# Kernel optimization log

Measured on AMD Instinct MI355X. Metric: run time of the kernel, lower is better.

Reference implementation:

```python
import jax, jax.numpy as jnp
import numpy as np

B, N, D = 16, 4096, 768   # bags, instances per bag, feature dim
H, L, K = 12, 2, 16       # heads, MHA layers, topk
DH = D // H               # head dim (also gate hidden dim)


def _ln(x, g, b, eps=1e-5):
    m = x.mean(-1, keepdims=True)
    v = x.var(-1, keepdims=True)
    return (x - m) / jnp.sqrt(v + eps) * g + b


def setup_inputs() -> dict:
    key = jax.random.key(0)
    ks = jax.random.split(key, 8)
    s = 0.02
    return {
        "x": jax.random.normal(ks[0], (B, N, D), jnp.float32),
        "cls_token": jax.random.normal(ks[1], (1, 1, D), jnp.float32),
        "ln_g": jnp.ones((D,), jnp.float32),
        "ln_b": jnp.zeros((D,), jnp.float32),
        "gln_g": jnp.ones((D,), jnp.float32),
        "gln_b": jnp.zeros((D,), jnp.float32),
        "gW1": jax.random.normal(ks[2], (DH, D), jnp.float32) * s,
        "gb1": jnp.zeros((DH,), jnp.float32),
        "gW2": jax.random.normal(ks[3], (1, DH), jnp.float32) * s,
        "gb2": jnp.zeros((1,), jnp.float32),
        "Wqkv": jax.random.normal(ks[4], (L, 3 * D, D), jnp.float32) * s,
        "bqkv": jnp.zeros((L, 3 * D), jnp.float32),
        "Wo": jax.random.normal(ks[5], (L, D, D), jnp.float32) * s,
        "bo": jnp.zeros((L, D), jnp.float32),
    }


def reference(x, cls_token, ln_g, ln_b, gln_g, gln_b, gW1, gb1, gW2, gb2, Wqkv, bqkv, Wo, bo):
    # --- per-bag attention gate: LN -> Linear(D,DH) -> GELU -> Linear(DH,1) -> sigmoid ---
    z = _ln(x, gln_g, gln_b)                                      # [B,N,D]
    h = jax.nn.gelu(jnp.einsum('bnd,ed->bne', z, gW1) + gb1, approximate=False)
    w = jax.nn.sigmoid((jnp.einsum('bne,oe->bno', h, gW2) + gb2)[..., 0])  # [B,N]
    # --- top-k selection (argsort descending, take first K) + gather + weight ---
    topv, topi = jax.lax.top_k(w, K)                              # [B,K]
    sel = jnp.take_along_axis(x, topi[..., None], axis=1) * topv[..., None]  # [B,K,D]
    # --- prepend cls token, shared LayerNorm ---
    cls = jnp.broadcast_to(cls_token, (B, 1, D))
    seq = jnp.concatenate([cls, sel], axis=1)                     # [B,K+1,D]
    z0 = _ln(seq, ln_g, ln_b)
    a = z0
    S = K + 1
    scale = 1.0 / jnp.sqrt(jnp.asarray(DH, jnp.float32))
    # --- stacked MHA; residual always from z0, shared ln (matches source) ---
    for l in range(L):
        qkv = jnp.einsum('bsd,ed->bse', a, Wqkv[l]) + bqkv[l]     # [B,S,3D]
        q, k, v = jnp.split(qkv, 3, axis=-1)
        q = q.reshape(B, S, H, DH)
        k = k.reshape(B, S, H, DH)
        v = v.reshape(B, S, H, DH)
        att = jax.nn.softmax(jnp.einsum('bqhd,bkhd->bhqk', q, k) * scale, axis=-1)
        o = jnp.einsum('bhqk,bkhd->bqhd', att, v).reshape(B, S, D)
        o = jnp.einsum('bsd,ed->bse', o, Wo[l]) + bo[l]
        a = _ln(z0 + o, ln_g, ln_b)
    # dropout is identity in eval mode
    return a[:, 0, :]                                             # [B,D]
```

## Files before the change

### kernel.cpp

```cpp
#include <hip/hip_runtime.h>
#include <hip/hip_bf16.h>
#include <math.h>

#define B_   16
#define N_   4096
#define D_   768
#define H_   12
#define L_   2
#define K_   16
#define S_   17
#define M_   272
#define BN_  65536

typedef __bf16 bf16x8 __attribute__((ext_vector_type(8)));
typedef float  f32x4  __attribute__((ext_vector_type(4)));

static __device__ __forceinline__ unsigned short f2bf(float f) {
    __bf16 h = (__bf16)f;
    return __builtin_bit_cast(unsigned short, h);
}
static __device__ __forceinline__ float bf2f(unsigned short u) {
    __bf16 h = __builtin_bit_cast(__bf16, u);
    return (float)h;
}
static __device__ __forceinline__ unsigned long long umax64(unsigned long long a, unsigned long long b) {
    return a > b ? a : b;
}

__global__ __launch_bounds__(256)
void gate_kernel(const float* __restrict__ x,
                 const float* __restrict__ gln_g,
                 const float* __restrict__ gln_b,
                 const float* __restrict__ gW1,
                 const float* __restrict__ gb1,
                 const float* __restrict__ gW2,
                 const float* __restrict__ gb2,
                 float* __restrict__ wbuf)
{
    __shared__ unsigned short smem[24576];
    unsigned short* Xh = smem;
    unsigned short* Xl = smem + 8192;
    unsigned short* Wh = smem + 16384;
    unsigned short* Wl = smem + 20480;
    char* XhB = (char*)Xh; char* XlB = (char*)Xl;
    char* WhB = (char*)Wh; char* WlB = (char*)Wl;

    const int t   = threadIdx.x;
    const int bn0 = blockIdx.x * 128;

    const int trow  = t >> 1;
    const int thalf = (t & 1) * 32;
    const int te    = t >> 2;
    const int tq    = (t & 3) * 16;

    const float* xrow = x + (size_t)(bn0 + trow) * D_ + thalf;
    const float* wrow = gW1 + (size_t)te * D_ + tq;

    const int wv = t >> 6;
    const int l  = t & 63;
    const int fr = l & 15;
    const int fq = l >> 4;

    f32x4 acc[2][4];
    #pragma unroll
    for (int mi = 0; mi < 2; ++mi)
        #pragma unroll
        for (int ni = 0; ni < 4; ++ni) {
            f32x4 z = {0.f, 0.f, 0.f, 0.f};
            acc[mi][ni] = z;
        }

    float sxp = 0.f, sxxp = 0.f;
    float a1p = 0.f, a2p = 0.f;

    for (int kt = 0; kt < 12; ++kt) {
        __syncthreads();
        const float* src = xrow + kt * 64;
        #pragma unroll
        for (int j = 0; j < 8; ++j) {
            float4 v = *(const float4*)(src + j * 4);
            sxp  += v.x + v.y + v.z + v.w;
            sxxp += v.x * v.x + v.y * v.y + v.z * v.z + v.w * v.w;
            ushort4 hh, ll;
            hh.x = f2bf(v.x); ll.x = f2bf(v.x - bf2f(hh.x));
            hh.y = f2bf(v.y); ll.y = f2bf(v.y - bf2f(hh.y));
            hh.z = f2bf(v.z); ll.z = f2bf(v.z - bf2f(hh.z));
            hh.w = f2bf(v.w); ll.w = f2bf(v.w - bf2f(hh.w));
            int byte = trow * 128 + (thalf + j * 4) * 2;
            int sw   = byte ^ ((trow & 7) << 4);
            *(ushort4*)(XhB + sw) = hh;
            *(ushort4*)(XlB + sw) = ll;
        }
        const float* wsrc = wrow + kt * 64;
        const float* gsrc = gln_g + kt * 64 + tq;
        const float* bsrc = gln_b + kt * 64 + tq;
        #pragma unroll
        for (int j = 0; j < 4; ++j) {
            float4 w4 = *(const float4*)(wsrc + j * 4);
            float4 g4 = *(const float4*)(gsrc + j * 4);
            float4 b4 = *(const float4*)(bsrc + j * 4);
            float4 wt;
            wt.x = w4.x * g4.x; wt.y = w4.y * g4.y;
            wt.z = w4.z * g4.z; wt.w = w4.w * g4.w;
            a1p += wt.x + wt.y + wt.z + wt.w;
            a2p += b4.x * w4.x + b4.y * w4.y + b4.z * w4.z + b4.w * w4.w;
            ushort4 hh, ll;
            hh.x = f2bf(wt.x); ll.x = f2bf(wt.x - bf2f(hh.x));
            hh.y = f2bf(wt.y); ll.y = f2bf(wt.y - bf2f(hh.y));
            hh.z = f2bf(wt.z); ll.z = f2bf(wt.z - bf2f(hh.z));
            hh.w = f2bf(wt.w); ll.w = f2bf(wt.w - bf2f(hh.w));
            int byte = te * 128 + (tq + j * 4) * 2;
            int sw   = byte ^ ((te & 7) << 4);
            *(ushort4*)(WhB + sw) = hh;
            *(ushort4*)(WlB + sw) = ll;
        }
        __syncthreads();
        #pragma unroll
        for (int ks = 0; ks < 2; ++ks) {
            int k0 = ks * 32 + fq * 8;
            bf16x8 ah[2], al[2], bh[4], bl[4];
            #pragma unroll
            for (int mi = 0; mi < 2; ++mi) {
                int r    = wv * 32 + mi * 16 + fr;
                int byte = (r * 128 + k0 * 2) ^ ((r & 7) << 4);
                ah[mi] = *(const bf16x8*)(XhB + byte);
                al[mi] = *(const bf16x8*)(XlB + byte);
            }
            #pragma unroll
            for (int ni = 0; ni < 4; ++ni) {
                int e    = ni * 16 + fr;
                int byte = (e * 128 + k0 * 2) ^ ((e & 7) << 4);
                bh[ni] = *(const bf16x8*)(WhB + byte);
                bl[ni] = *(const bf16x8*)(WlB + byte);
            }
            #pragma unroll
            for (int mi = 0; mi < 2; ++mi)
                #pragma unroll
                for (int ni = 0; ni < 4; ++ni) {
                    acc[mi][ni] = __builtin_amdgcn_mfma_f32_16x16x32_bf16(ah[mi], bh[ni], acc[mi][ni], 0, 0, 0);
                    acc[mi][ni] = __builtin_amdgcn_mfma_f32_16x16x32_bf16(ah[mi], bl[ni], acc[mi][ni], 0, 0, 0);
                    acc[mi][ni] = __builtin_amdgcn_mfma_f32_16x16x32_bf16(al[mi], bh[ni], acc[mi][ni], 0, 0, 0);
                }
        }
    }
    __syncthreads();

    float* F    = (float*)smem;
    float* mS   = F;
    float* rS   = F + 128;
    float* A1s  = F + 256;
    float* A2s  = F + 320;
    float* redS = F + 384;
    float* redQ = F + 640;
    float* rA1  = F + 896;
    float* rA2  = F + 1152;

    redS[trow * 2 + (t & 1)] = sxp;
    redQ[trow * 2 + (t & 1)] = sxxp;
    rA1[te * 4 + (t & 3)] = a1p;
    rA2[te * 4 + (t & 3)] = a2p;
    __syncthreads();
    if (t < 128) {
        float s = redS[t * 2] + redS[t * 2 + 1];
        float q = redQ[t * 2] + redQ[t * 2 + 1];
        float m = s * (1.0f / D_);
        mS[t] = m;
        rS[t] = rsqrtf(q * (1.0f / D_) - m * m + 1e-5f);
    }
    if (t < 64) {
        A1s[t] = rA1[t * 4] + rA1[t * 4 + 1] + rA1[t * 4 + 2] + rA1[t * 4 + 3];
        A2s[t] = rA2[t * 4] + rA2[t * 4 + 1] + rA2[t * 4 + 2] + rA2[t * 4 + 3];
    }
    __syncthreads();

    float w2v[4], a1v[4], a2b[4];
    #pragma unroll
    for (int ni = 0; ni < 4; ++ni) {
        int e = ni * 16 + fr;
        w2v[ni] = gW2[e];
        a1v[ni] = A1s[e];
        a2b[ni] = A2s[e] + gb1[e];
    }
    float gb2v = gb2[0];

    #pragma unroll
    for (int mi = 0; mi < 2; ++mi) {
        #pragma unroll
        for (int j = 0; j < 4; ++j) {
            int inst = wv * 32 + mi * 16 + fq * 4 + j;
            float m = mS[inst], rs = rS[inst];
            float tp = 0.f;
            #pragma unroll
            for (int ni = 0; ni < 4; ++ni) {
                float h  = rs * (acc[mi][ni][j] - m * a1v[ni]) + a2b[ni];
                float hg = 0.5f * h * (1.0f + erff(h * 0.70710678118654752f));
                tp = fmaf(hg, w2v[ni], tp);
            }
            tp += __shfl_xor(tp, 1);
            tp += __shfl_xor(tp, 2);
            tp += __shfl_xor(tp, 4);
            tp += __shfl_xor(tp, 8);
            if (fr == 0) wbuf[bn0 + inst] = 1.0f / (1.0f + expf(-(tp + gb2v)));
        }
    }
}

__global__ __launch_bounds__(1024)
void topk_kernel(const float* __restrict__ wbuf,
                 float* __restrict__ topv, int* __restrict__ topi)
{
    const int b = blockIdx.x, t = threadIdx.x;
    const int lane = t & 63, wid = t >> 6;
    __shared__ unsigned long long wred[16];
    __shared__ unsigned long long winkey;

    unsigned long long key[4];
    float4 v = *(const float4*)&wbuf[(size_t)b * N_ + t * 4];
    key[0] = ((unsigned long long)__float_as_uint(v.x) << 12) | (unsigned long long)(4095 - (t * 4 + 0));
    key[1] = ((unsigned long long)__float_as_uint(v.y) << 12) | (unsigned long long)(4095 - (t * 4 + 1));
    key[2] = ((unsigned long long)__float_as_uint(v.z) << 12) | (unsigned long long)(4095 - (t * 4 + 2));
    key[3] = ((unsigned long long)__float_as_uint(v.w) << 12) | (unsigned long long)(4095 - (t * 4 + 3));

    for (int k = 0; k < K_; ++k) {
        unsigned long long kk = umax64(umax64(key[0], key[1]), umax64(key[2], key[3]));
        #pragma unroll
        for (int o = 1; o < 64; o <<= 1) kk = umax64(kk, (unsigned long long)__shfl_xor(kk, o));
        if (lane == 0) wred[wid] = kk;
        __syncthreads();
        if (t == 0) {
            unsigned long long m = wred[0];
            #pragma unroll
            for (int i = 1; i < 16; ++i) m = umax64(m, wred[i]);
            winkey = m;
            int wi = 4095 - (int)(m & 0xfffULL);
            topv[b * K_ + k] = __uint_as_float((unsigned int)(m >> 12));
            topi[b * K_ + k] = wi;
        }
        __syncthreads();
        unsigned long long m = winkey;
        int wi = 4095 - (int)(m & 0xfffULL);
        if ((wi >> 2) == t) key[wi & 3] = 0ULL;
    }
}

__global__ __launch_bounds__(256)
void build_kernel(const float* __restrict__ x, const float* __restrict__ cls,
                  const float* __restrict__ ln_g, const float* __restrict__ ln_b,
                  const float* __restrict__ topv, const int* __restrict__ topi,
                  float* __restrict__ z0, float* __restrict__ abuf)
{
    const int r = blockIdx.x, b = r / S_, s = r % S_;
    __shared__ float sm[8];
    float v[3];
    if (s == 0) {
        #pragma unroll
        for (int p = 0; p < 3; ++p) v[p] = cls[threadIdx.x + 256 * p];
    } else {
        int   idx = topi[b * K_ + s - 1];
        float tv  = topv[b * K_ + s - 1];
        const float* row = &x[((size_t)b * N_ + idx) * D_];
        #pragma unroll
        for (int p = 0; p < 3; ++p) v[p] = row[threadIdx.x + 256 * p] * tv;
    }
    float sum = 0.f, ss = 0.f;
    #pragma unroll
    for (int p = 0; p < 3; ++p) { sum += v[p]; ss += v[p] * v[p]; }
    #pragma unroll
    for (int o = 32; o; o >>= 1) { sum += __shfl_down(sum, o); ss += __shfl_down(ss, o); }
    int wid = threadIdx.x >> 6, lane = threadIdx.x & 63;
    if (lane == 0) { sm[wid * 2] = sum; sm[wid * 2 + 1] = ss; }
    __syncthreads();
    sum = sm[0] + sm[2] + sm[4] + sm[6];
    ss  = sm[1] + sm[3] + sm[5] + sm[7];
    float m = sum * (1.0f / D_), rstd = rsqrtf(ss * (1.0f / D_) - m * m + 1e-5f);
    #pragma unroll
    for (int p = 0; p < 3; ++p) {
        int d = threadIdx.x + 256 * p;
        float z = (v[p] - m) * rstd * ln_g[d] + ln_b[d];
        z0[(size_t)r * D_ + d]   = z;
        abuf[(size_t)r * D_ + d] = z;
    }
}

__global__ __launch_bounds__(256)
void gemm_mfma(const float* __restrict__ A, const float* __restrict__ W,
               const float* __restrict__ bias, float* __restrict__ C, int N)
{
    __shared__ unsigned short smem[16384];
    char* AhB = (char*)smem;
    char* AlB = (char*)(smem + 4096);
    char* WhB = (char*)(smem + 8192);
    char* WlB = (char*)(smem + 12288);

    const int t  = threadIdx.x;
    const int m0 = blockIdx.x * 64, n0 = blockIdx.y * 64;

    const int sr = t >> 2;
    const int sc = (t & 3) * 16;
    const int gm = m0 + sr;
    const bool aok = (gm < M_);
    const float* asrc = A + (size_t)gm * D_ + sc;
    const float* wsrc = W + (size_t)(n0 + sr) * D_ + sc;

    const int wv = t >> 6, l = t & 63;
    const int fr = l & 15, fq = l >> 4;
    const int wm = (wv & 1) * 32, wn = (wv >> 1) * 32;

    f32x4 acc[2][2];
    #pragma unroll
    for (int mi = 0; mi < 2; ++mi)
        #pragma unroll
        for (int ni = 0; ni < 2; ++ni) {
            f32x4 z = {0.f, 0.f, 0.f, 0.f};
            acc[mi][ni] = z;
        }

    float4 pa[4], pw[4];
    #pragma unroll
    for (int q = 0; q < 4; ++q) {
        pa[q] = aok ? *(const float4*)(asrc + q * 4) : make_float4(0.f, 0.f, 0.f, 0.f);
        pw[q] = *(const float4*)(wsrc + q * 4);
    }

    const int abyte0 = sr * 128 + sc * 2;
    const int asw0   = (abyte0)      ^ ((sr & 7) << 4);
    const int asw1   = (abyte0 + 16) ^ ((sr & 7) << 4);

    for (int kt = 0; kt < 12; ++kt) {
        __syncthreads();
        {
            ushort4 hh[4], ll[4];
            #pragma unroll
            for (int q = 0; q < 4; ++q) {
                hh[q].x = f2bf(pa[q].x); ll[q].x = f2bf(pa[q].x - bf2f(hh[q].x));
                hh[q].y = f2bf(pa[q].y); ll[q].y = f2bf(pa[q].y - bf2f(hh[q].y));
                hh[q].z = f2bf(pa[q].z); ll[q].z = f2bf(pa[q].z - bf2f(hh[q].z));
                hh[q].w = f2bf(pa[q].w); ll[q].w = f2bf(pa[q].w - bf2f(hh[q].w));
            }
            *(ushort4*)(AhB + asw0)     = hh[0];
            *(ushort4*)(AhB + asw0 + 8) = hh[1];
            *(ushort4*)(AhB + asw1)     = hh[2];
            *(ushort4*)(AhB + asw1 + 8) = hh[3];
            *(ushort4*)(AlB + asw0)     = ll[0];
            *(ushort4*)(AlB + asw0 + 8) = ll[1];
            *(ushort4*)(AlB + asw1)     = ll[2];
            *(ushort4*)(AlB + asw1 + 8) = ll[3];
            #pragma unroll
            for (int q = 0; q < 4; ++q) {
                hh[q].x = f2bf(pw[q].x); ll[q].x = f2bf(pw[q].x - bf2f(hh[q].x));
                hh[q].y = f2bf(pw[q].y); ll[q].y = f2bf(pw[q].y - bf2f(hh[q].y));
                hh[q].z = f2bf(pw[q].z); ll[q].z = f2bf(pw[q].z - bf2f(hh[q].z));
                hh[q].w = f2bf(pw[q].w); ll[q].w = f2bf(pw[q].w - bf2f(hh[q].w));
            }
            *(ushort4*)(WhB + asw0)     = hh[0];
            *(ushort4*)(WhB + asw0 + 8) = hh[1];
            *(ushort4*)(WhB + asw1)     = hh[2];
            *(ushort4*)(WhB + asw1 + 8) = hh[3];
            *(ushort4*)(WlB + asw0)     = ll[0];
            *(ushort4*)(WlB + asw0 + 8) = ll[1];
            *(ushort4*)(WlB + asw1)     = ll[2];
            *(ushort4*)(WlB + asw1 + 8) = ll[3];
        }
        __syncthreads();
        if (kt < 11) {
            const float* an = asrc + (kt + 1) * 64;
            const float* wn2 = wsrc + (kt + 1) * 64;
            #pragma unroll
            for (int q = 0; q < 4; ++q) {
                pa[q] = aok ? *(const float4*)(an + q * 4) : make_float4(0.f, 0.f, 0.f, 0.f);
                pw[q] = *(const float4*)(wn2 + q * 4);
            }
        }
        #pragma unroll
        for (int ks = 0; ks < 2; ++ks) {
            int kb = ks * 64 + fq * 16;
            bf16x8 ah[2], al[2], bh[2], bl[2];
            #pragma unroll
            for (int mi = 0; mi < 2; ++mi) {
                int r    = wm + mi * 16 + fr;
                int byte = (r * 128 + kb) ^ ((r & 7) << 4);
                ah[mi] = *(const bf16x8*)(AhB + byte);
                al[mi] = *(const bf16x8*)(AlB + byte);
            }
            #pragma unroll
            for (int ni = 0; ni < 2; ++ni) {
                int r    = wn + ni * 16 + fr;
                int byte = (r * 128 + kb) ^ ((r & 7) << 4);
                bh[ni] = *(const bf16x8*)(WhB + byte);
                bl[ni] = *(const bf16x8*)(WlB + byte);
            }
            #pragma unroll
            for (int mi = 0; mi < 2; ++mi)
                #pragma unroll
                for (int ni = 0; ni < 2; ++ni) {
                    acc[mi][ni] = __builtin_amdgcn_mfma_f32_16x16x32_bf16(ah[mi], bh[ni], acc[mi][ni], 0, 0, 0);
                    acc[mi][ni] = __builtin_amdgcn_mfma_f32_16x16x32_bf16(ah[mi], bl[ni], acc[mi][ni], 0, 0, 0);
                    acc[mi][ni] = __builtin_amdgcn_mfma_f32_16x16x32_bf16(al[mi], bh[ni], acc[mi][ni], 0, 0, 0);
                }
        }
    }

    #pragma unroll
    for (int mi = 0; mi < 2; ++mi) {
        #pragma unroll
        for (int j = 0; j < 4; ++j) {
            int m = m0 + wm + mi * 16 + fq * 4 + j;
            if (m < M_) {
                #pragma unroll
                for (int ni = 0; ni < 2; ++ni) {
                    int n = n0 + wn + ni * 16 + fr;
                    C[(size_t)m * N + n] = acc[mi][ni][j] + bias[n];
                }
            }
        }
    }
}

__global__ __launch_bounds__(128)
void attn_kernel(const float* __restrict__ qkv, float* __restrict__ obuf)
{
    __shared__ float qs[S_][65], ks[S_][65], vs[S_][65], att[S_][18];
    const int bh = blockIdx.x, b = bh / H_, h = bh % H_;
    const int bq = b * S_;
    const int tid = threadIdx.x;

    for (int idx = tid; idx < S_ * 64; idx += 128) {
        int s = idx >> 6, d = idx & 63;
        size_t off = (size_t)(bq + s) * (3 * D_) + h * 64 + d;
        qs[s][d] = qkv[off];
        ks[s][d] = qkv[off + D_];
        vs[s][d] = qkv[off + 2 * D_];
    }
    __syncthreads();
    for (int t = tid; t < S_ * S_; t += 128) {
        int i = t / S_, j = t % S_;
        float sdot = 0.f;
        #pragma unroll
        for (int d = 0; d < 64; ++d) sdot = fmaf(qs[i][d], ks[j][d], sdot);
        att[i][j] = sdot * 0.125f;
    }
    __syncthreads();
    if (tid < S_) {
        float mx = -1e30f;
        for (int j = 0; j < S_; ++j) mx = fmaxf(mx, att[tid][j]);
        float ssum = 0.f;
        for (int j = 0; j < S_; ++j) { float e = expf(att[tid][j] - mx); att[tid][j] = e; ssum += e; }
        float inv = 1.0f / ssum;
        for (int j = 0; j < S_; ++j) att[tid][j] *= inv;
    }
    __syncthreads();
    for (int t = tid; t < S_ * 64; t += 128) {
        int i = t >> 6, d = t & 63;
        float s = 0.f;
        #pragma unroll
        for (int j = 0; j < S_; ++j) s = fmaf(att[i][j], vs[j][d], s);
        obuf[(size_t)(bq + i) * D_ + h * 64 + d] = s;
    }
}

__global__ __launch_bounds__(256)
void resln_kernel(const float* __restrict__ z0, const float* __restrict__ proj,
                  const float* __restrict__ ln_g, const float* __restrict__ ln_b,
                  float* __restrict__ abuf, float* __restrict__ dout, int writeOut)
{
    const int r = blockIdx.x;
    __shared__ float sm[8];
    float v[3];
    #pragma unroll
    for (int p = 0; p < 3; ++p) {
        int d = threadIdx.x + 256 * p;
        v[p] = z0[(size_t)r * D_ + d] + proj[(size_t)r * D_ + d];
    }
    float sum = 0.f, ss = 0.f;
    #pragma unroll
    for (int p = 0; p < 3; ++p) { sum += v[p]; ss += v[p] * v[p]; }
    #pragma unroll
    for (int o = 32; o; o >>= 1) { sum += __shfl_down(sum, o); ss += __shfl_down(ss, o); }
    int wid = threadIdx.x >> 6, lane = threadIdx.x & 63;
    if (lane == 0) { sm[wid * 2] = sum; sm[wid * 2 + 1] = ss; }
    __syncthreads();
    sum = sm[0] + sm[2] + sm[4] + sm[6];
    ss  = sm[1] + sm[3] + sm[5] + sm[7];
    float m = sum * (1.0f / D_), rstd = rsqrtf(ss * (1.0f / D_) - m * m + 1e-5f);
    #pragma unroll
    for (int p = 0; p < 3; ++p) {
        int d = threadIdx.x + 256 * p;
        float a = (v[p] - m) * rstd * ln_g[d] + ln_b[d];
        abuf[(size_t)r * D_ + d] = a;
        if (writeOut && (r % S_) == 0) dout[(size_t)(r / S_) * D_ + d] = a;
    }
}

extern "C" void kernel_launch(void* const* d_in, const int* in_sizes, int n_in,
                              void* d_out, int out_size, void* d_ws, size_t ws_size,
                              hipStream_t stream)
{
    const float* x     = (const float*)d_in[0];
    const float* cls   = (const float*)d_in[1];
    const float* ln_g  = (const float*)d_in[2];
    const float* ln_b  = (const float*)d_in[3];
    const float* gln_g = (const float*)d_in[4];
    const float* gln_b = (const float*)d_in[5];
    const float* gW1   = (const float*)d_in[6];
    const float* gb1   = (const float*)d_in[7];
    const float* gW2   = (const float*)d_in[8];
    const float* gb2   = (const float*)d_in[9];
    const float* Wqkv  = (const float*)d_in[10];
    const float* bqkv  = (const float*)d_in[11];
    const float* Wo    = (const float*)d_in[12];
    const float* bo    = (const float*)d_in[13];
    float* out = (float*)d_out;

    float* ws   = (float*)d_ws;
    float* wbuf = ws;
    float* topv = ws + BN_;
    int*   topi = (int*)(ws + BN_ + 256);
    float* z0   = ws + BN_ + 512;
    float* abuf = z0 + (size_t)M_ * D_;
    float* qkvb = abuf + (size_t)M_ * D_;
    float* obuf = qkvb + (size_t)M_ * 3 * D_;
    float* projb = obuf + (size_t)M_ * D_;

    gate_kernel<<<BN_ / 128, 256, 0, stream>>>(x, gln_g, gln_b, gW1, gb1, gW2, gb2, wbuf);
    topk_kernel<<<B_, 1024, 0, stream>>>(wbuf, topv, topi);
    build_kernel<<<M_, 256, 0, stream>>>(x, cls, ln_g, ln_b, topv, topi, z0, abuf);
    for (int l = 0; l < L_; ++l) {
        gemm_mfma<<<dim3(5, 36), 256, 0, stream>>>(abuf, Wqkv + (size_t)l * 3 * D_ * D_,
                                                   bqkv + (size_t)l * 3 * D_, qkvb, 3 * D_);
        attn_kernel<<<B_ * H_, 128, 0, stream>>>(qkvb, obuf);
        gemm_mfma<<<dim3(5, 12), 256, 0, stream>>>(obuf, Wo + (size_t)l * D_ * D_,
                                                   bo + (size_t)l * D_, projb, D_);
        resln_kernel<<<M_, 256, 0, stream>>>(z0, projb, ln_g, ln_b, abuf, out,
                                             (l == L_ - 1) ? 1 : 0);
    }
}
```

Measured before the change: 187.0 us.

## Fuse all stages into one cooperative persistent kernel with grid syncs

Replaces the chain of eleven kernel launches with a single cooperative kernel of 256 blocks that runs gate, top-k, build, and both MHA layers, separating stages with grid.sync(). Top-k is rewritten for 256 threads holding 16 keys each, and attention now uses 256 threads. The aim is to remove launch gaps and tail idle time between the small stages. In exchange the gate stage runs on fewer blocks, each doing two tiles in sequence, and grid-wide barriers add their own cost. A fallback path with separate kernels is kept.

Result: faster. 180.4 us (-3.5%).

```diff
diff --git a/kernel.cpp b/kernel.cpp
--- a/kernel.cpp
+++ b/kernel.cpp
@@ -1,6 +1,9 @@
 #include <hip/hip_runtime.h>
 #include <hip/hip_bf16.h>
+#include <hip/hip_cooperative_groups.h>
 #include <math.h>
+
+namespace cg = cooperative_groups;
 
 #define B_   16
 #define N_   4096
@@ -11,6 +14,7 @@
 #define S_   17
 #define M_   272
 #define BN_  65536
+#define GRID_ 256
 
 typedef __bf16 bf16x8 __attribute__((ext_vector_type(8)));
 typedef float  f32x4  __attribute__((ext_vector_type(4)));
@@ -27,26 +31,19 @@
     return a > b ? a : b;
 }
 
-__global__ __launch_bounds__(256)
-void gate_kernel(const float* __restrict__ x,
-                 const float* __restrict__ gln_g,
-                 const float* __restrict__ gln_b,
-                 const float* __restrict__ gW1,
-                 const float* __restrict__ gb1,
-                 const float* __restrict__ gW2,
-                 const float* __restrict__ gb2,
-                 float* __restrict__ wbuf)
-{
-    __shared__ unsigned short smem[24576];
-    unsigned short* Xh = smem;
-    unsigned short* Xl = smem + 8192;
-    unsigned short* Wh = smem + 16384;
-    unsigned short* Wl = smem + 20480;
-    char* XhB = (char*)Xh; char* XlB = (char*)Xl;
-    char* WhB = (char*)Wh; char* WlB = (char*)Wl;
-
-    const int t   = threadIdx.x;
-    const int bn0 = blockIdx.x * 128;
+
+static __device__ __forceinline__
+void gate_block(unsigned short* smem,
+                const float* __restrict__ x,  const float* __restrict__ gln_g,
+                const float* __restrict__ gln_b, const float* __restrict__ gW1,
+                const float* __restrict__ gb1, const float* __restrict__ gW2,
+                const float* __restrict__ gb2, float* __restrict__ wbuf,
+                int bn0, int t)
+{
+    char* XhB = (char*)(smem);
+    char* XlB = (char*)(smem + 8192);
+    char* WhB = (char*)(smem + 16384);
+    char* WlB = (char*)(smem + 20480);
 
     const int trow  = t >> 1;
     const int thalf = (t & 1) * 32;
@@ -57,9 +54,9 @@
     const float* wrow = gW1 + (size_t)te * D_ + tq;
 
     const int wv = t >> 6;
-    const int l  = t & 63;
-    const int fr = l & 15;
-    const int fq = l >> 4;
+    const int la = t & 63;
+    const int fr = la & 15;
+    const int fq = la >> 4;
 
     f32x4 acc[2][4];
     #pragma unroll
@@ -205,95 +202,94 @@
     }
 }
 
-__global__ __launch_bounds__(1024)
-void topk_kernel(const float* __restrict__ wbuf,
-                 float* __restrict__ topv, int* __restrict__ topi)
-{
-    const int b = blockIdx.x, t = threadIdx.x;
-    const int lane = t & 63, wid = t >> 6;
-    __shared__ unsigned long long wred[16];
-    __shared__ unsigned long long winkey;
-
-    unsigned long long key[4];
-    float4 v = *(const float4*)&wbuf[(size_t)b * N_ + t * 4];
-    key[0] = ((unsigned long long)__float_as_uint(v.x) << 12) | (unsigned long long)(4095 - (t * 4 + 0));
-    key[1] = ((unsigned long long)__float_as_uint(v.y) << 12) | (unsigned long long)(4095 - (t * 4 + 1));
-    key[2] = ((unsigned long long)__float_as_uint(v.z) << 12) | (unsigned long long)(4095 - (t * 4 + 2));
-    key[3] = ((unsigned long long)__float_as_uint(v.w) << 12) | (unsigned long long)(4095 - (t * 4 + 3));
-
+static __device__ __forceinline__
+void topk_block(unsigned long long* SB, const float* __restrict__ wbuf,
+                float* __restrict__ topv, int* __restrict__ topi, int b, int t)
+{
+    unsigned long long* wred   = SB;
+    unsigned long long* winkey = SB + 8;
+    const int la = t & 63, wid = t >> 6;
+
+    unsigned long long key[16];
+    #pragma unroll
+    for (int j = 0; j < 16; ++j) {
+        int i = t + 256 * j;
+        float v = wbuf[(size_t)b * N_ + i];
+        key[j] = ((unsigned long long)__float_as_uint(v) << 12) | (unsigned long long)(4095 - i);
+    }
     for (int k = 0; k < K_; ++k) {
-        unsigned long long kk = umax64(umax64(key[0], key[1]), umax64(key[2], key[3]));
+        unsigned long long kk = key[0];
+        #pragma unroll
+        for (int j = 1; j < 16; ++j) kk = umax64(kk, key[j]);
         #pragma unroll
         for (int o = 1; o < 64; o <<= 1) kk = umax64(kk, (unsigned long long)__shfl_xor(kk, o));
-        if (lane == 0) wred[wid] = kk;
+        if (la == 0) wred[wid] = kk;
         __syncthreads();
         if (t == 0) {
-            unsigned long long m = wred[0];
-            #pragma unroll
-            for (int i = 1; i < 16; ++i) m = umax64(m, wred[i]);
-            winkey = m;
+            unsigned long long m = umax64(umax64(wred[0], wred[1]), umax64(wred[2], wred[3]));
+            *winkey = m;
             int wi = 4095 - (int)(m & 0xfffULL);
             topv[b * K_ + k] = __uint_as_float((unsigned int)(m >> 12));
             topi[b * K_ + k] = wi;
         }
         __syncthreads();
-        unsigned long long m = winkey;
+        unsigned long long m = *winkey;
         int wi = 4095 - (int)(m & 0xfffULL);
-        if ((wi >> 2) == t) key[wi & 3] = 0ULL;
-    }
-}
-
-__global__ __launch_bounds__(256)
-void build_kernel(const float* __restrict__ x, const float* __restrict__ cls,
-                  const float* __restrict__ ln_g, const float* __restrict__ ln_b,
-                  const float* __restrict__ topv, const int* __restrict__ topi,
-                  float* __restrict__ z0, float* __restrict__ abuf)
-{
-    const int r = blockIdx.x, b = r / S_, s = r % S_;
-    __shared__ float sm[8];
+        #pragma unroll
+        for (int j = 0; j < 16; ++j)
+            if (wi == t + 256 * j) key[j] = 0ULL;
+        __syncthreads();
+    }
+}
+
+static __device__ __forceinline__
+void build_row(float* sm, const float* __restrict__ x, const float* __restrict__ cls,
+               const float* __restrict__ ln_g, const float* __restrict__ ln_b,
+               const float* __restrict__ topv, const int* __restrict__ topi,
+               float* __restrict__ z0, float* __restrict__ abuf, int r, int t)
+{
+    const int b = r / S_, s = r % S_;
     float v[3];
     if (s == 0) {
         #pragma unroll
-        for (int p = 0; p < 3; ++p) v[p] = cls[threadIdx.x + 256 * p];
+        for (int p = 0; p < 3; ++p) v[p] = cls[t + 256 * p];
     } else {
         int   idx = topi[b * K_ + s - 1];
         float tv  = topv[b * K_ + s - 1];
         const float* row = &x[((size_t)b * N_ + idx) * D_];
         #pragma unroll
-        for (int p = 0; p < 3; ++p) v[p] = row[threadIdx.x + 256 * p] * tv;
+        for (int p = 0; p < 3; ++p) v[p] = row[t + 256 * p] * tv;
     }
     float sum = 0.f, ss = 0.f;
     #pragma unroll
     for (int p = 0; p < 3; ++p) { sum += v[p]; ss += v[p] * v[p]; }
     #pragma unroll
     for (int o = 32; o; o >>= 1) { sum += __shfl_down(sum, o); ss += __shfl_down(ss, o); }
-    int wid = threadIdx.x >> 6, lane = threadIdx.x & 63;
-    if (lane == 0) { sm[wid * 2] = sum; sm[wid * 2 + 1] = ss; }
+    int wid = t >> 6, la = t & 63;
+    if (la == 0) { sm[wid * 2] = sum; sm[wid * 2 + 1] = ss; }
     __syncthreads();
     sum = sm[0] + sm[2] + sm[4] + sm[6];
     ss  = sm[1] + sm[3] + sm[5] + sm[7];
+    __syncthreads();
     float m = sum * (1.0f / D_), rstd = rsqrtf(ss * (1.0f / D_) - m * m + 1e-5f);
     #pragma unroll
     for (int p = 0; p < 3; ++p) {
-        int d = threadIdx.x + 256 * p;
+        int d = t + 256 * p;
         float z = (v[p] - m) * rstd * ln_g[d] + ln_b[d];
         z0[(size_t)r * D_ + d]   = z;
         abuf[(size_t)r * D_ + d] = z;
     }
 }
 
-__global__ __launch_bounds__(256)
-void gemm_mfma(const float* __restrict__ A, const float* __restrict__ W,
-               const float* __restrict__ bias, float* __restrict__ C, int N)
-{
-    __shared__ unsigned short smem[16384];
-    char* AhB = (char*)smem;
-    char* AlB = (char*)(smem + 4096);
-    char* WhB = (char*)(smem + 8192);
-    char* WlB = (char*)(smem + 12288);
-
-    const int t  = threadIdx.x;
-    const int m0 = blockIdx.x * 64, n0 = blockIdx.y * 64;
+static __device__ __forceinline__
+void gemm_stage(char* SB, const float* __restrict__ A, const float* __restrict__ W,
+                const float* __restrict__ bias, float* __restrict__ C, int N,
+                int m0, int n0, int t)
+{
+    char* AhB = SB;
+    char* AlB = SB + 8192;
+    char* WhB = SB + 16384;
+    char* WlB = SB + 24576;
 
     const int sr = t >> 2;
     const int sc = (t & 3) * 16;
@@ -302,8 +298,8 @@
     const float* asrc = A + (size_t)gm * D_ + sc;
     const float* wsrc = W + (size_t)(n0 + sr) * D_ + sc;
 
-    const int wv = t >> 6, l = t & 63;
-    const int fr = l & 15, fq = l >> 4;
+    const int wv = t >> 6, la = t & 63;
+    const int fr = la & 15, fq = la >> 4;
     const int wm = (wv & 1) * 32, wn = (wv >> 1) * 32;
 
     f32x4 acc[2][2];
@@ -363,7 +359,7 @@
         }
         __syncthreads();
         if (kt < 11) {
-            const float* an = asrc + (kt + 1) * 64;
+            const float* an  = asrc + (kt + 1) * 64;
             const float* wn2 = wsrc + (kt + 1) * 64;
             #pragma unroll
             for (int q = 0; q < 4; ++q) {
@@ -416,79 +412,189 @@
     }
 }
 
-__global__ __launch_bounds__(128)
-void attn_kernel(const float* __restrict__ qkv, float* __restrict__ obuf)
-{
-    __shared__ float qs[S_][65], ks[S_][65], vs[S_][65], att[S_][18];
-    const int bh = blockIdx.x, b = bh / H_, h = bh % H_;
+static __device__ __forceinline__
+void attn_block(float* F, const float* __restrict__ qkvb, float* __restrict__ obuf,
+                int bh, int t)
+{
+    float* qs  = F;
+    float* ks  = F + S_ * 65;
+    float* vs  = F + 2 * S_ * 65;
+    float* att = F + 3 * S_ * 65;
+    const int b = bh / H_, h = bh % H_;
     const int bq = b * S_;
-    const int tid = threadIdx.x;
-
-    for (int idx = tid; idx < S_ * 64; idx += 128) {
+    for (int idx = t; idx < S_ * 64; idx += 256) {
         int s = idx >> 6, d = idx & 63;
         size_t off = (size_t)(bq + s) * (3 * D_) + h * 64 + d;
-        qs[s][d] = qkv[off];
-        ks[s][d] = qkv[off + D_];
-        vs[s][d] = qkv[off + 2 * D_];
-    }
-    __syncthreads();
-    for (int t = tid; t < S_ * S_; t += 128) {
-        int i = t / S_, j = t % S_;
+        qs[s * 65 + d] = qkvb[off];
+        ks[s * 65 + d] = qkvb[off + D_];
+        vs[s * 65 + d] = qkvb[off + 2 * D_];
+    }
+    __syncthreads();
+    for (int idx = t; idx < S_ * S_; idx += 256) {
+        int i = idx / S_, j = idx % S_;
         float sdot = 0.f;
         #pragma unroll
-        for (int d = 0; d < 64; ++d) sdot = fmaf(qs[i][d], ks[j][d], sdot);
-        att[i][j] = sdot * 0.125f;
-    }
-    __syncthreads();
-    if (tid < S_) {
+        for (int d = 0; d < 64; ++d) sdot = fmaf(qs[i * 65 + d], ks[j * 65 + d], sdot);
+        att[i * 18 + j] = sdot * 0.125f;
+    }
+    __syncthreads();
+    if (t < S_) {
         float mx = -1e30f;
-        for (int j = 0; j < S_; ++j) mx = fmaxf(mx, att[tid][j]);
+        for (int j = 0; j < S_; ++j) mx = fmaxf(mx, att[t * 18 + j]);
         float ssum = 0.f;
-        for (int j = 0; j < S_; ++j) { float e = expf(att[tid][j] - mx); att[tid][j] = e; ssum += e; }
+        for (int j = 0; j < S_; ++j) { float e = expf(att[t * 18 + j] - mx); att[t * 18 + j] = e; ssum += e; }
         float inv = 1.0f / ssum;
-        for (int j = 0; j < S_; ++j) att[tid][j] *= inv;
-    }
-    __syncthreads();
-    for (int t = tid; t < S_ * 64; t += 128) {
-        int i = t >> 6, d = t & 63;
+        for (int j = 0; j < S_; ++j) att[t * 18 + j] *= inv;
+    }
+    __syncthreads();
+    for (int idx = t; idx < S_ * 64; idx += 256) {
+        int i = idx >> 6, d = idx & 63;
         float s = 0.f;
         #pragma unroll
-        for (int j = 0; j < S_; ++j) s = fmaf(att[i][j], vs[j][d], s);
+        for (int j = 0; j < S_; ++j) s = fmaf(att[i * 18 + j], vs[j * 65 + d], s);
         obuf[(size_t)(bq + i) * D_ + h * 64 + d] = s;
     }
 }
 
-__global__ __launch_bounds__(256)
-void resln_kernel(const float* __restrict__ z0, const float* __restrict__ proj,
-                  const float* __restrict__ ln_g, const float* __restrict__ ln_b,
-                  float* __restrict__ abuf, float* __restrict__ dout, int writeOut)
-{
-    const int r = blockIdx.x;
-    __shared__ float sm[8];
+static __device__ __forceinline__
+void resln_row(float* sm, const float* __restrict__ z0, const float* __restrict__ projb,
+               const float* __restrict__ ln_g, const float* __restrict__ ln_b,
+               float* __restrict__ abuf, float* __restrict__ out, int r, int t, int writeOut)
+{
     float v[3];
     #pragma unroll
     for (int p = 0; p < 3; ++p) {
-        int d = threadIdx.x + 256 * p;
-        v[p] = z0[(size_t)r * D_ + d] + proj[(size_t)r * D_ + d];
+        int d = t + 256 * p;
+        v[p] = z0[(size_t)r * D_ + d] + projb[(size_t)r * D_ + d];
     }
     float sum = 0.f, ss = 0.f;
     #pragma unroll
     for (int p = 0; p < 3; ++p) { sum += v[p]; ss += v[p] * v[p]; }
     #pragma unroll
     for (int o = 32; o; o >>= 1) { sum += __shfl_down(sum, o); ss += __shfl_down(ss, o); }
-    int wid = threadIdx.x >> 6, lane = threadIdx.x & 63;
-    if (lane == 0) { sm[wid * 2] = sum; sm[wid * 2 + 1] = ss; }
+    int wid = t >> 6, la = t & 63;
+    if (la == 0) { sm[wid * 2] = sum; sm[wid * 2 + 1] = ss; }
     __syncthreads();
     sum = sm[0] + sm[2] + sm[4] + sm[6];
     ss  = sm[1] + sm[3] + sm[5] + sm[7];
+    __syncthreads();
     float m = sum * (1.0f / D_), rstd = rsqrtf(ss * (1.0f / D_) - m * m + 1e-5f);
     #pragma unroll
     for (int p = 0; p < 3; ++p) {
-        int d = threadIdx.x + 256 * p;
+        int d = t + 256 * p;
         float a = (v[p] - m) * rstd * ln_g[d] + ln_b[d];
         abuf[(size_t)r * D_ + d] = a;
-        if (writeOut && (r % S_) == 0) dout[(size_t)(r / S_) * D_ + d] = a;
-    }
+        if (writeOut && (r % S_) == 0) out[(size_t)(r / S_) * D_ + d] = a;
+    }
+}
+
+__global__ __launch_bounds__(256)
+void fused_kernel(const float* __restrict__ x, const float* __restrict__ cls,
+                  const float* __restrict__ ln_g, const float* __restrict__ ln_b,
+                  const float* __restrict__ gln_g, const float* __restrict__ gln_b,
+                  const float* __restrict__ gW1, const float* __restrict__ gb1,
+                  const float* __restrict__ gW2, const float* __restrict__ gb2,
+                  const float* __restrict__ Wqkv, const float* __restrict__ bqkv,
+                  const float* __restrict__ Wo, const float* __restrict__ bo,
+                  float* out,
+                  float* wbuf, float* topv, int* topi,
+                  float* z0, float* abuf, float* qkvb, float* obuf, float* projb)
+{
+    cg::grid_group grid = cg::this_grid();
+    __shared__ __align__(16) char SMEM[49152];
+    const int bid = blockIdx.x;
+    const int t   = threadIdx.x;
+
+    #pragma unroll 1
+    for (int half = 0; half < 2; ++half)
+        gate_block((unsigned short*)SMEM, x, gln_g, gln_b, gW1, gb1, gW2, gb2,
+                   wbuf, bid * 256 + half * 128, t);
+    grid.sync();
+
+    if (bid < B_) topk_block((unsigned long long*)SMEM, wbuf, topv, topi, bid, t);
+    grid.sync();
+
+    #pragma unroll 1
+    for (int r = bid; r < M_; r += GRID_)
+        build_row((float*)SMEM, x, cls, ln_g, ln_b, topv, topi, z0, abuf, r, t);
+    grid.sync();
+
+    #pragma unroll 1
+    for (int l = 0; l < L_; ++l) {
+        if (bid < 180)
+            gemm_stage(SMEM, abuf, Wqkv + (size_t)l * 3 * D_ * D_,
+                       bqkv + (size_t)l * 3 * D_, qkvb, 3 * D_,
+                       (bid / 36) * 64, (bid % 36) * 64, t);
+        grid.sync();
+
+        if (bid < B_ * H_) attn_block((float*)SMEM, qkvb, obuf, bid, t);
+        grid.sync();
+
+        if (bid < 60)
+            gemm_stage(SMEM, obuf, Wo + (size_t)l * D_ * D_,
+                       bo + (size_t)l * D_, projb, D_,
+                       (bid / 12) * 64, (bid % 12) * 64, t);
+        grid.sync();
+
+        #pragma unroll 1
+        for (int r = bid; r < M_; r += GRID_)
+            resln_row((float*)SMEM, z0, projb, ln_g, ln_b, abuf, out, r, t,
+                      (l == L_ - 1) ? 1 : 0);
+        if (l == 0) grid.sync();
+    }
+}
+
+__global__ __launch_bounds__(256)
+void gate_kernel(const float* __restrict__ x, const float* __restrict__ gln_g,
+                 const float* __restrict__ gln_b, const float* __restrict__ gW1,
+                 const float* __restrict__ gb1, const float* __restrict__ gW2,
+                 const float* __restrict__ gb2, float* __restrict__ wbuf)
+{
+    __shared__ __align__(16) unsigned short smem[24576];
+    gate_block(smem, x, gln_g, gln_b, gW1, gb1, gW2, gb2, wbuf,
+               blockIdx.x * 128, threadIdx.x);
+}
+
+__global__ __launch_bounds__(256)
+void topk_kernel(const float* __restrict__ wbuf, float* __restrict__ topv,
+                 int* __restrict__ topi)
+{
+    __shared__ unsigned long long SB[16];
+    topk_block(SB, wbuf, topv, topi, blockIdx.x, threadIdx.x);
+}
+
+__global__ __launch_bounds__(256)
+void build_kernel(const float* __restrict__ x, const float* __restrict__ cls,
+                  const float* __restrict__ ln_g, const float* __restrict__ ln_b,
+                  const float* __restrict__ topv, const int* __restrict__ topi,
+                  float* __restrict__ z0, float* __restrict__ abuf)
+{
+    __shared__ float sm[8];
+    build_row(sm, x, cls, ln_g, ln_b, topv, topi, z0, abuf, blockIdx.x, threadIdx.x);
+}
+
+__global__ __launch_bounds__(256)
+void gemm_mfma(const float* __restrict__ A, const float* __restrict__ W,
+               const float* __restrict__ bias, float* __restrict__ C, int N)
+{
+    __shared__ __align__(16) char SB[32768];
+    gemm_stage(SB, A, W, bias, C, N, blockIdx.x * 64, blockIdx.y * 64, threadIdx.x);
+}
+
+__global__ __launch_bounds__(256)
+void attn_kernel(const float* __restrict__ qkvb, float* __restrict__ obuf)
+{
+    __shared__ __align__(16) float F[3 * S_ * 65 + S_ * 18];
+    attn_block(F, qkvb, obuf, blockIdx.x, threadIdx.x);
+}
+
+__global__ __launch_bounds__(256)
+void resln_kernel(const float* __restrict__ z0, const float* __restrict__ projb,
+                  const float* __restrict__ ln_g, const float* __restrict__ ln_b,
+                  float* __restrict__ abuf, float* __restrict__ out, int writeOut)
+{
+    __shared__ float sm[8];
+    resln_row(sm, z0, projb, ln_g, ln_b, abuf, out, blockIdx.x, threadIdx.x, writeOut);
 }
 
 extern "C" void kernel_launch(void* const* d_in, const int* in_sizes, int n_in,
@@ -521,16 +627,33 @@
     float* obuf = qkvb + (size_t)M_ * 3 * D_;
     float* projb = obuf + (size_t)M_ * D_;
 
-    gate_kernel<<<BN_ / 128, 256, 0, stream>>>(x, gln_g, gln_b, gW1, gb1, gW2, gb2, wbuf);
-    topk_kernel<<<B_, 1024, 0, stream>>>(wbuf, topv, topi);
-    build_kernel<<<M_, 256, 0, stream>>>(x, cls, ln_g, ln_b, topv, topi, z0, abuf);
-    for (int l = 0; l < L_; ++l) {
-        gemm_mfma<<<dim3(5, 36), 256, 0, stream>>>(abuf, Wqkv + (size_t)l * 3 * D_ * D_,
-                                                   bqkv + (size_t)l * 3 * D_, qkvb, 3 * D_);
-        attn_kernel<<<B_ * H_, 128, 0, stream>>>(qkvb, obuf);
-        gemm_mfma<<<dim3(5, 12), 256, 0, stream>>>(obuf, Wo + (size_t)l * D_ * D_,
-                                                   bo + (size_t)l * D_, projb, D_);
-        resln_kernel<<<M_, 256, 0, stream>>>(z0, projb, ln_g, ln_b, abuf, out,
-                                             (l == L_ - 1) ? 1 : 0);
-    }
-}
+    hipError_t lerr = hipErrorUnknown;
+    int nb = 0;
+    if (hipOccupancyMaxActiveBlocksPerMultiprocessor(
+            &nb, (const void*)fused_kernel, 256, 0) == hipSuccess && nb >= 1) {
+        void* args[] = {
+            (void*)&x, (void*)&cls, (void*)&ln_g, (void*)&ln_b,
+            (void*)&gln_g, (void*)&gln_b, (void*)&gW1, (void*)&gb1,
+            (void*)&gW2, (void*)&gb2, (void*)&Wqkv, (void*)&bqkv,
+            (void*)&Wo, (void*)&bo, (void*)&out,
+            (void*)&wbuf, (void*)&topv, (void*)&topi,
+            (void*)&z0, (void*)&abuf, (void*)&qkvb, (void*)&obuf, (void*)&projb
+        };
+        lerr = hipLaunchCooperativeKernel((const void*)fused_kernel, dim3(GRID_),
+                                          dim3(256), args, 0, stream);
+    }
+    if (lerr != hipSuccess) {
+        gate_kernel<<<BN_ / 128, 256, 0, stream>>>(x, gln_g, gln_b, gW1, gb1, gW2, gb2, wbuf);
+        topk_kernel<<<B_, 256, 0, stream>>>(wbuf, topv, topi);
+        build_kernel<<<M_, 256, 0, stream>>>(x, cls, ln_g, ln_b, topv, topi, z0, abuf);
+        for (int l = 0; l < L_; ++l) {
+            gemm_mfma<<<dim3(5, 36), 256, 0, stream>>>(abuf, Wqkv + (size_t)l * 3 * D_ * D_,
+                                                       bqkv + (size_t)l * 3 * D_, qkvb, 3 * D_);
+            attn_kernel<<<B_ * H_, 256, 0, stream>>>(qkvb, obuf);
+            gemm_mfma<<<dim3(5, 12), 256, 0, stream>>>(obuf, Wo + (size_t)l * D_ * D_,
+                                                       bo + (size_t)l * D_, projb, D_);
+            resln_kernel<<<M_, 256, 0, stream>>>(z0, projb, ln_g, ln_b, abuf, out,
+                                                 (l == L_ - 1) ? 1 : 0);
+        }
+    }
+}
```
